# Performance work log

Measured on AMD Instinct MI355X. Metric: run time of the kernel, lower is better.

Reference implementation:

```python
import jax, jax.numpy as jnp
import numpy as np

N_NODES = 50000
N_EDGES = 500000
ATOM_DIM = 128
BOND_DIM = 64
EMB = 128
N_GRAPHS = 256
NUM_LAYER = 2


def _kaiming_uniform(key, fan_out, fan_in):
    # kaiming_uniform_ with nonlinearity='relu': bound = sqrt(6 / fan_in) * sqrt(2)/1 adjustments
    gain = np.sqrt(2.0)
    bound = gain * np.sqrt(3.0 / fan_in)
    return jax.random.uniform(key, (fan_out, fan_in), jnp.float32, -bound, bound)


def setup_inputs() -> dict:
    key = jax.random.key(0)
    ks = jax.random.split(key, 12)
    x = jax.random.normal(ks[0], (N_NODES, ATOM_DIM), jnp.float32)
    edge_attr = jax.random.normal(ks[1], (N_EDGES, BOND_DIM), jnp.float32)
    edge_index = jax.random.randint(ks[2], (2, N_EDGES), 0, N_NODES, jnp.int64)
    batch = jnp.sort(jax.random.randint(ks[3], (N_NODES,), 0, N_GRAPHS, jnp.int64))
    Wa = _kaiming_uniform(ks[4], EMB, ATOM_DIM)
    ba = jnp.zeros((EMB,), jnp.float32)
    Wb = _kaiming_uniform(ks[5], EMB, BOND_DIM)
    bb = jnp.zeros((EMB,), jnp.float32)
    W1 = _kaiming_uniform(ks[6], EMB, EMB)
    b1 = jnp.zeros((EMB,), jnp.float32)
    W2 = _kaiming_uniform(ks[7], EMB // 2, EMB)
    b2 = jnp.zeros((EMB // 2,), jnp.float32)
    W3 = _kaiming_uniform(ks[8], 1, EMB // 2)
    return {"x": x, "edge_attr": edge_attr, "edge_index": edge_index, "batch": batch,
            "Wa": Wa, "ba": ba, "Wb": Wb, "bb": bb,
            "W1": W1, "b1": b1, "W2": W2, "b2": b2, "W3": W3}


def reference(x, edge_attr, edge_index, batch, Wa, ba, Wb, bb, W1, b1, W2, b2, W3):
    src, dst = edge_index[0], edge_index[1]
    # Step 1: embeddings
    node_emb = x @ Wa.T + ba          # [N, EMB]
    edge_emb = edge_attr @ Wb.T + bb  # [E, EMB]
    # Step 2: message passing layers: gather, multiply with edge_emb, scatter-add, residual
    for _ in range(NUM_LAYER):
        msg = node_emb[src] * edge_emb                           # [E, EMB]
        agg = jax.ops.segment_sum(msg, dst, num_segments=N_NODES)  # [N, EMB]
        node_emb = node_emb + agg
    # Step 3: energy MLP (ReLU first, per nn.Sequential)
    h = jax.nn.relu(node_emb)
    h = jax.nn.relu(h @ W1.T + b1)
    h = jax.nn.relu(h @ W2.T + b2)
    node_energy = h @ W3.T            # [N, 1], no bias
    # Step 4: global add pool over graphs
    dg = jax.ops.segment_sum(node_energy, batch, num_segments=N_GRAPHS)  # [G, 1]
    return dg
```

## Files before the change

### kernel.cpp

```cpp
#include <hip/hip_runtime.h>
#include <cstdio>
#include <cstdint>

#define N_NODES 50000
#define N_EDGES 500000
#define EMB 128
#define BOND 64
#define NGRAPH 256
#define NB_SCAN ((N_NODES + 255) / 256)
#define NSTRIP (N_NODES / 16)
#define HSTR 136

typedef short bf16x8 __attribute__((ext_vector_type(8)));
typedef float f32x4  __attribute__((ext_vector_type(4)));

__device__ __forceinline__ unsigned short f2bf(float v){
  unsigned u = __float_as_uint(v);
  unsigned r = (u + 0x7fffu + ((u >> 16) & 1u)) >> 16;
  return (unsigned short)r;
}
__device__ __forceinline__ float bf2f(unsigned short u){
  return __uint_as_float(((unsigned)u) << 16);
}
__device__ __forceinline__ unsigned short brelu(unsigned short u){
  return (u & 0x8000u) ? (unsigned short)0 : u;
}

__global__ void prep_w(const float* __restrict__ Wa, const float* __restrict__ W1,
                       const float* __restrict__ W2, unsigned short* __restrict__ wabf,
                       unsigned short* __restrict__ w1bf, unsigned short* __restrict__ w2bf)
{
  int i = blockIdx.x * 256 + threadIdx.x;
  int i2 = i & 16383;
  int j = i2 & 7, lb = (i2 >> 3) & 63, kc = (i2 >> 9) & 3, tn = i2 >> 11;
  int lm = lb & 15, q = lb >> 4;
  int row = tn * 16 + lm, col = kc * 32 + q * 8 + j;
  if (i < 16384){
    wabf[i] = f2bf(Wa[row * EMB + col]);
  } else if (i < 32768){
    w1bf[i2] = f2bf(W1[row * EMB + col]);
  } else if (i < 32768 + 8192){
    w2bf[i2] = f2bf(W2[row * EMB + col]);
  }
}

__global__ __launch_bounds__(256) void node_gemm_mfma(const float* __restrict__ x,
    const unsigned short* __restrict__ wabf, const float* __restrict__ ba,
    unsigned short* __restrict__ out)
{
  __shared__ unsigned short hs[4][16 * HSTR];
  const int t = threadIdx.x;
  const int wv = t >> 6, l = t & 63;
  const int lm = l & 15, q = l >> 4;
  union U8 { bf16x8 v; unsigned short s[8]; };
  const int strip = blockIdx.x * 4 + wv;
  if (strip >= NSTRIP) return;
  const long n0 = (long)strip * 16;

  bf16x8 a[4];
  #pragma unroll
  for (int kc = 0; kc < 4; kc++){
    const float* ap = x + (n0 + lm) * (long)EMB + kc * 32 + q * 8;
    float4 x0 = *(const float4*)ap;
    float4 x1 = *(const float4*)(ap + 4);
    U8 u;
    u.s[0] = f2bf(x0.x); u.s[1] = f2bf(x0.y); u.s[2] = f2bf(x0.z); u.s[3] = f2bf(x0.w);
    u.s[4] = f2bf(x1.x); u.s[5] = f2bf(x1.y); u.s[6] = f2bf(x1.z); u.s[7] = f2bf(x1.w);
    a[kc] = u.v;
  }
  float biasv[8];
  #pragma unroll
  for (int tn = 0; tn < 8; tn++) biasv[tn] = ba[tn * 16 + lm];

  unsigned short* hw = hs[wv];
  #pragma unroll
  for (int tn = 0; tn < 8; tn++){
    f32x4 acc = {0.f, 0.f, 0.f, 0.f};
    #pragma unroll
    for (int kc = 0; kc < 4; kc++){
      bf16x8 bf = *(const bf16x8*)(wabf + (size_t)((tn * 4 + kc) * 64 + l) * 8);
      acc = __builtin_amdgcn_mfma_f32_16x16x32_bf16(a[kc], bf, acc, 0, 0, 0);
    }
    #pragma unroll
    for (int i = 0; i < 4; i++)
      hw[(q * 4 + i) * HSTR + tn * 16 + lm] = f2bf(acc[i] + biasv[tn]);
  }
  #pragma unroll
  for (int rb = 0; rb < 4; rb++){
    int row = rb * 4 + q;
    ushort4 v0 = *(const ushort4*)(hw + row * HSTR + lm * 8);
    ushort4 v1 = *(const ushort4*)(hw + row * HSTR + lm * 8 + 4);
    unsigned short* op = out + (n0 + row) * (long)EMB + lm * 8;
    *(ushort4*)op = v0;
    *(ushort4*)(op + 4) = v1;
  }
}

__global__ __launch_bounds__(128) void edge_gemm_mfma(
    const float* __restrict__ attr, const float* __restrict__ Wb,
    const float* __restrict__ bb, const int2* __restrict__ cse,
    unsigned short* __restrict__ eemb)
{
  __shared__ unsigned short hs[2][32 * HSTR];
  const int t = threadIdx.x;
  const int wv = t >> 6;
  const int l  = t & 63;
  const int lm = l & 15;
  const int q  = l >> 4;
  union U8 { bf16x8 v; unsigned short s[8]; };

  bf16x8 bfrag[8][2];
  float bias[8];
  #pragma unroll
  for (int tn = 0; tn < 8; tn++){
    bias[tn] = bb[tn * 16 + lm];
    #pragma unroll
    for (int h = 0; h < 2; h++){
      const float* wp = Wb + (tn * 16 + lm) * BOND + h * 32 + q * 8;
      float4 w0 = *(const float4*)wp;
      float4 w1 = *(const float4*)(wp + 4);
      U8 u;
      u.s[0] = f2bf(w0.x); u.s[1] = f2bf(w0.y); u.s[2] = f2bf(w0.z); u.s[3] = f2bf(w0.w);
      u.s[4] = f2bf(w1.x); u.s[5] = f2bf(w1.y); u.s[6] = f2bf(w1.z); u.s[7] = f2bf(w1.w);
      bfrag[tn][h] = u.v;
    }
  }

  unsigned short* hw = hs[wv];
  const long stride = (long)gridDim.x * 2 * 32;
  for (long p0 = ((long)blockIdx.x * 2 + wv) * 32; p0 < N_EDGES; p0 += stride){
    long eidA = (long)cse[p0 + lm].y;
    long eidB = (long)cse[p0 + 16 + lm].y;
    bf16x8 afA[2], afB[2];
    #pragma unroll
    for (int h = 0; h < 2; h++){
      const float* apA = attr + eidA * BOND + h * 32 + q * 8;
      const float* apB = attr + eidB * BOND + h * 32 + q * 8;
      float4 a0 = *(const float4*)apA;
      float4 a1 = *(const float4*)(apA + 4);
      float4 b0 = *(const float4*)apB;
      float4 b1 = *(const float4*)(apB + 4);
      U8 u;
      u.s[0] = f2bf(a0.x); u.s[1] = f2bf(a0.y); u.s[2] = f2bf(a0.z); u.s[3] = f2bf(a0.w);
      u.s[4] = f2bf(a1.x); u.s[5] = f2bf(a1.y); u.s[6] = f2bf(a1.z); u.s[7] = f2bf(a1.w);
      afA[h] = u.v;
      u.s[0] = f2bf(b0.x); u.s[1] = f2bf(b0.y); u.s[2] = f2bf(b0.z); u.s[3] = f2bf(b0.w);
      u.s[4] = f2bf(b1.x); u.s[5] = f2bf(b1.y); u.s[6] = f2bf(b1.z); u.s[7] = f2bf(b1.w);
      afB[h] = u.v;
    }
    #pragma unroll
    for (int tn = 0; tn < 8; tn++){
      f32x4 accA = {0.f, 0.f, 0.f, 0.f};
      f32x4 accB = {0.f, 0.f, 0.f, 0.f};
      accA = __builtin_amdgcn_mfma_f32_16x16x32_bf16(afA[0], bfrag[tn][0], accA, 0, 0, 0);
      accA = __builtin_amdgcn_mfma_f32_16x16x32_bf16(afA[1], bfrag[tn][1], accA, 0, 0, 0);
      accB = __builtin_amdgcn_mfma_f32_16x16x32_bf16(afB[0], bfrag[tn][0], accB, 0, 0, 0);
      accB = __builtin_amdgcn_mfma_f32_16x16x32_bf16(afB[1], bfrag[tn][1], accB, 0, 0, 0);
      #pragma unroll
      for (int i = 0; i < 4; i++){
        hw[(q * 4 + i) * HSTR + tn * 16 + lm]      = f2bf(accA[i] + bias[tn]);
        hw[(16 + q * 4 + i) * HSTR + tn * 16 + lm] = f2bf(accB[i] + bias[tn]);
      }
    }
    #pragma unroll
    for (int rb = 0; rb < 8; rb++){
      int row = rb * 4 + q;
      ushort4 v0 = *(const ushort4*)(hw + row * HSTR + lm * 8);
      ushort4 v1 = *(const ushort4*)(hw + row * HSTR + lm * 8 + 4);
      unsigned short* op = eemb + (p0 + row) * (long)EMB + lm * 8;
      *(ushort4*)op = v0;
      *(ushort4*)(op + 4) = v1;
    }
  }
}


__global__ __launch_bounds__(256) void count_deg(const int* __restrict__ ei,
                                                 int* __restrict__ deg)
{
  int e = blockIdx.x * 256 + threadIdx.x;
  if (e < N_EDGES) atomicAdd(&deg[ei[N_EDGES + e]], 1);
}

__global__ __launch_bounds__(256) void scan_s1(const int* __restrict__ deg,
                                               int* __restrict__ blocksum)
{
  int i = blockIdx.x * 256 + threadIdx.x;
  int lane = threadIdx.x & 63, w = threadIdx.x >> 6;
  int v = (i < N_NODES) ? deg[i] : 0;
  #pragma unroll
  for (int o = 32; o > 0; o >>= 1) v += __shfl_down(v, o, 64);
  __shared__ int ws4[4];
  if (lane == 0) ws4[w] = v;
  __syncthreads();
  if (threadIdx.x == 0) blocksum[blockIdx.x] = ws4[0] + ws4[1] + ws4[2] + ws4[3];
}

__global__ __launch_bounds__(256) void scan_s2(const int* __restrict__ blocksum,
                                               int* __restrict__ blockoff,
                                               int* __restrict__ off)
{
  int t = threadIdx.x;
  int lane = t & 63, w = t >> 6;
  int v = (t < NB_SCAN) ? blocksum[t] : 0;
  int x = v;
  #pragma unroll
  for (int d = 1; d < 64; d <<= 1){
    int y = __shfl_up(x, d, 64);
    if (lane >= d) x += y;
  }
  __shared__ int wsum[4];
  if (lane == 63) wsum[w] = x;
  __syncthreads();
  int wo = 0;
  for (int j = 0; j < w; j++) wo += wsum[j];
  if (t < NB_SCAN) blockoff[t] = wo + x - v;
  if (t == 0) off[N_NODES] = wsum[0] + wsum[1] + wsum[2] + wsum[3];
}

__global__ __launch_bounds__(256) void scan_s3(const int* __restrict__ deg,
    const int* __restrict__ blockoff, int* __restrict__ off, int* __restrict__ fill)
{
  int i = blockIdx.x * 256 + threadIdx.x;
  int lane = threadIdx.x & 63, w = threadIdx.x >> 6;
  int v = (i < N_NODES) ? deg[i] : 0;
  int x = v;
  #pragma unroll
  for (int d = 1; d < 64; d <<= 1){
    int y = __shfl_up(x, d, 64);
    if (lane >= d) x += y;
  }
  __shared__ int wsum[4];
  if (lane == 63) wsum[w] = x;
  __syncthreads();
  int wo = 0;
  for (int j = 0; j < w; j++) wo += wsum[j];
  if (i < N_NODES){
    int excl = blockoff[blockIdx.x] + wo + x - v;
    off[i] = excl;
    fill[i] = excl;
  }
}

__global__ __launch_bounds__(256) void scatter_edges(const int* __restrict__ ei,
    int* __restrict__ fill, int2* __restrict__ cse)
{
  int e = blockIdx.x * 256 + threadIdx.x;
  if (e < N_EDGES){
    int dst = ei[N_EDGES + e];
    int p = atomicAdd(&fill[dst], 1);
    cse[p] = make_int2(ei[e], e);
  }
}

__global__ __launch_bounds__(256) void agg_kernel(const unsigned short* __restrict__ node_old,
    const unsigned short* __restrict__ eemb, const int* __restrict__ off,
    const int2* __restrict__ cse, unsigned short* __restrict__ node_new)
{
  int n = blockIdx.x * 8 + (threadIdx.x >> 5);
  if (n >= N_NODES) return;
  int c0 = (threadIdx.x & 31) * 4;
  int s = off[n], e = off[n + 1];
  ushort4 r = *(const ushort4*)(node_old + (long)n * EMB + c0);
  float4 accA = make_float4(bf2f(r.x), bf2f(r.y), bf2f(r.z), bf2f(r.w));
  float4 accB = make_float4(0.f, 0.f, 0.f, 0.f);
  int i = s;
  for (; i + 8 <= e; i += 8){
    int idx[8];
    #pragma unroll
    for (int j = 0; j < 8; j++) idx[j] = cse[i + j].x;
    ushort4 a[8], eb[8];
    #pragma unroll
    for (int j = 0; j < 8; j++){
      a[j]  = *(const ushort4*)(node_old + (long)idx[j] * EMB + c0);
      eb[j] = *(const ushort4*)(eemb + (long)(i + j) * EMB + c0);
    }
    #pragma unroll
    for (int j = 0; j < 8; j++){
      float4& acc = (j & 1) ? accB : accA;
      acc.x = fmaf(bf2f(a[j].x), bf2f(eb[j].x), acc.x);
      acc.y = fmaf(bf2f(a[j].y), bf2f(eb[j].y), acc.y);
      acc.z = fmaf(bf2f(a[j].z), bf2f(eb[j].z), acc.z);
      acc.w = fmaf(bf2f(a[j].w), bf2f(eb[j].w), acc.w);
    }
  }
  for (; i < e; i++){
    int src = cse[i].x;
    ushort4 a  = *(const ushort4*)(node_old + (long)src * EMB + c0);
    ushort4 eb = *(const ushort4*)(eemb + (long)i * EMB + c0);
    accA.x = fmaf(bf2f(a.x), bf2f(eb.x), accA.x);
    accA.y = fmaf(bf2f(a.y), bf2f(eb.y), accA.y);
    accA.z = fmaf(bf2f(a.z), bf2f(eb.z), accA.z);
    accA.w = fmaf(bf2f(a.w), bf2f(eb.w), accA.w);
  }
  ushort4 o;
  o.x = f2bf(accA.x + accB.x);
  o.y = f2bf(accA.y + accB.y);
  o.z = f2bf(accA.z + accB.z);
  o.w = f2bf(accA.w + accB.w);
  *(ushort4*)(node_new + (long)n * EMB + c0) = o;
}

__global__ __launch_bounds__(256) void mlp_mfma_pool(const unsigned short* __restrict__ ne,
    const unsigned short* __restrict__ w1bf, const unsigned short* __restrict__ w2bf,
    const float* __restrict__ b1, const float* __restrict__ b2,
    const float* __restrict__ W3, const int* __restrict__ batch,
    float* __restrict__ dg)
{
  __shared__ float h1s[4][16 * 132];
  __shared__ float pool[NGRAPH];
  const int t = threadIdx.x;
  const int wv = t >> 6, l = t & 63;
  const int lm = l & 15, q = l >> 4;
  union U8 { bf16x8 v; unsigned short s[8]; };

  for (int i = t; i < NGRAPH; i += 256) pool[i] = 0.f;
  __syncthreads();

  const int strip = blockIdx.x * 4 + wv;
  if (strip < NSTRIP){
    const long n0 = (long)strip * 16;

    float b1v[8], b2v[4], w3v[4];
    #pragma unroll
    for (int tn = 0; tn < 8; tn++) b1v[tn] = b1[tn * 16 + lm];
    #pragma unroll
    for (int tc = 0; tc < 4; tc++){ b2v[tc] = b2[tc * 16 + lm]; w3v[tc] = W3[tc * 16 + lm]; }

    bf16x8 a1[4];
    #pragma unroll
    for (int kc = 0; kc < 4; kc++){
      const unsigned short* ap = ne + (n0 + lm) * (long)EMB + kc * 32 + q * 8;
      ushort4 v0 = *(const ushort4*)ap;
      ushort4 v1 = *(const ushort4*)(ap + 4);
      U8 u;
      u.s[0] = brelu(v0.x); u.s[1] = brelu(v0.y); u.s[2] = brelu(v0.z); u.s[3] = brelu(v0.w);
      u.s[4] = brelu(v1.x); u.s[5] = brelu(v1.y); u.s[6] = brelu(v1.z); u.s[7] = brelu(v1.w);
      a1[kc] = u.v;
    }

    f32x4 acc1[8];
    #pragma unroll
    for (int tn = 0; tn < 8; tn++) acc1[tn] = (f32x4){b1v[tn], b1v[tn], b1v[tn], b1v[tn]};
    #pragma unroll
    for (int kc = 0; kc < 4; kc++){
      #pragma unroll
      for (int tn = 0; tn < 8; tn++){
        bf16x8 bf = *(const bf16x8*)(w1bf + (size_t)((tn * 4 + kc) * 64 + l) * 8);
        acc1[tn] = __builtin_amdgcn_mfma_f32_16x16x32_bf16(a1[kc], bf, acc1[tn], 0, 0, 0);
      }
    }

    float* h1 = h1s[wv];
    #pragma unroll
    for (int tn = 0; tn < 8; tn++)
      #pragma unroll
      for (int i = 0; i < 4; i++)
        h1[(q * 4 + i) * 132 + tn * 16 + lm] = fmaxf(acc1[tn][i], 0.f);
    bf16x8 a2[4];
    #pragma unroll
    for (int kc = 0; kc < 4; kc++){
      const float* hp = h1 + lm * 132 + kc * 32 + q * 8;
      float4 x0 = *(const float4*)hp;
      float4 x1 = *(const float4*)(hp + 4);
      U8 u;
      u.s[0] = f2bf(x0.x); u.s[1] = f2bf(x0.y); u.s[2] = f2bf(x0.z); u.s[3] = f2bf(x0.w);
      u.s[4] = f2bf(x1.x); u.s[5] = f2bf(x1.y); u.s[6] = f2bf(x1.z); u.s[7] = f2bf(x1.w);
      a2[kc] = u.v;
    }

    f32x4 acc2[4];
    #pragma unroll
    for (int tc = 0; tc < 4; tc++) acc2[tc] = (f32x4){b2v[tc], b2v[tc], b2v[tc], b2v[tc]};
    #pragma unroll
    for (int kc = 0; kc < 4; kc++){
      #pragma unroll
      for (int tc = 0; tc < 4; tc++){
        bf16x8 bf = *(const bf16x8*)(w2bf + (size_t)((tc * 4 + kc) * 64 + l) * 8);
        acc2[tc] = __builtin_amdgcn_mfma_f32_16x16x32_bf16(a2[kc], bf, acc2[tc], 0, 0, 0);
      }
    }

    float e4[4];
    #pragma unroll
    for (int i = 0; i < 4; i++){
      float s = 0.f;
      #pragma unroll
      for (int tc = 0; tc < 4; tc++) s = fmaf(fmaxf(acc2[tc][i], 0.f), w3v[tc], s);
      e4[i] = s;
    }
    #pragma unroll
    for (int m = 1; m < 16; m <<= 1)
      #pragma unroll
      for (int i = 0; i < 4; i++) e4[i] += __shfl_xor(e4[i], m, 64);
    if (lm == 0){
      #pragma unroll
      for (int i = 0; i < 4; i++){
        int node = (int)n0 + q * 4 + i;
        atomicAdd(&pool[batch[node]], e4[i]);
      }
    }
  }
  __syncthreads();
  for (int i = t; i < NGRAPH; i += 256){
    float v = pool[i];
    if (v != 0.f) atomicAdd(&dg[i], v);
  }
}

extern "C" void kernel_launch(void* const* d_in, const int* in_sizes, int n_in,
                              void* d_out, int out_size, void* d_ws, size_t ws_size,
                              hipStream_t stream)
{
  const float* x         = (const float*)d_in[0];
  const float* edge_attr = (const float*)d_in[1];
  const int*   ei        = (const int*)d_in[2];
  const int*   batch     = (const int*)d_in[3];
  const float* Wa = (const float*)d_in[4];
  const float* ba = (const float*)d_in[5];
  const float* Wb = (const float*)d_in[6];
  const float* bb = (const float*)d_in[7];
  const float* W1 = (const float*)d_in[8];
  const float* b1 = (const float*)d_in[9];
  const float* W2 = (const float*)d_in[10];
  const float* b2 = (const float*)d_in[11];
  const float* W3 = (const float*)d_in[12];

  char* ws = (char*)d_ws;
  size_t p = 0;
  auto alloc = [&](size_t bytes) -> char* {
    char* q = ws + p;
    p += (bytes + 255) & ~(size_t)255;
    return q;
  };
  unsigned short* bufA = (unsigned short*)alloc((size_t)N_NODES * EMB * 2);
  unsigned short* bufB = (unsigned short*)alloc((size_t)N_NODES * EMB * 2);
  unsigned short* eemb = (unsigned short*)alloc((size_t)N_EDGES * EMB * 2);
  unsigned short* wabf = (unsigned short*)alloc(16384 * sizeof(short));
  unsigned short* w1bf = (unsigned short*)alloc(16384 * sizeof(short));
  unsigned short* w2bf = (unsigned short*)alloc(8192 * sizeof(short));
  int* deg  = (int*)alloc(N_NODES * sizeof(int));
  int* off  = (int*)alloc((N_NODES + 1) * sizeof(int));
  int* fill = (int*)alloc(N_NODES * sizeof(int));
  int* blocksum = (int*)alloc(NB_SCAN * sizeof(int));
  int* blockoff = (int*)alloc(NB_SCAN * sizeof(int));
  int2* cse = (int2*)alloc((size_t)N_EDGES * sizeof(int2));
  if (p > ws_size){
    fprintf(stderr, "kernel_launch: ws too small (%zu < %zu)\n", ws_size, p);
    return;
  }

  hipMemsetAsync(deg, 0, N_NODES * sizeof(int), stream);
  count_deg<<<(N_EDGES + 255) / 256, 256, 0, stream>>>(ei, deg);
  scan_s1<<<NB_SCAN, 256, 0, stream>>>(deg, blocksum);
  scan_s2<<<1, 256, 0, stream>>>(blocksum, blockoff, off);
  scan_s3<<<NB_SCAN, 256, 0, stream>>>(deg, blockoff, off, fill);
  scatter_edges<<<(N_EDGES + 255) / 256, 256, 0, stream>>>(ei, fill, cse);

  prep_w<<<160, 256, 0, stream>>>(Wa, W1, W2, wabf, w1bf, w2bf);
  node_gemm_mfma<<<(NSTRIP + 3) / 4, 256, 0, stream>>>(x, wabf, ba, bufA);
  edge_gemm_mfma<<<2048, 128, 0, stream>>>(edge_attr, Wb, bb, cse, eemb);

  agg_kernel<<<(N_NODES + 7) / 8, 256, 0, stream>>>(bufA, eemb, off, cse, bufB);
  agg_kernel<<<(N_NODES + 7) / 8, 256, 0, stream>>>(bufB, eemb, off, cse, bufA);

  hipMemsetAsync(d_out, 0, NGRAPH * sizeof(float), stream);
  mlp_mfma_pool<<<(NSTRIP + 3) / 4, 256, 0, stream>>>(bufA, w1bf, w2bf, b1, b2, W3, batch, (float*)d_out);
}
```

Baseline: 434.4 us.

## Store embeddings in permuted column order to drop LDS transpose staging

The node and edge GEMM kernels now write MFMA accumulators straight to global memory as 16-byte vectors. Each lane packs its 8 column tiles, so stored embeddings use a permuted column order. W1 is pre-permuted in prep_w to match, and the elementwise gather/multiply/scatter in aggregation is unaffected by the permutation. This removes the per-wave shared-memory round trip and its LDS traffic. The edge GEMM also loads a pre-converted bf16 Wb and processes 16 edges per wave with 4 waves per block, which trades per-wave reuse for more parallelism.

```diff
diff --git a/kernel.cpp b/kernel.cpp
--- a/kernel.cpp
+++ b/kernel.cpp
@@ -9,7 +9,7 @@
 #define NGRAPH 256
 #define NB_SCAN ((N_NODES + 255) / 256)
 #define NSTRIP (N_NODES / 16)
-#define HSTR 136
+#define ESTRIP (N_EDGES / 16)
 
 typedef short bf16x8 __attribute__((ext_vector_type(8)));
 typedef float f32x4  __attribute__((ext_vector_type(4)));
@@ -26,21 +26,31 @@
   return (u & 0x8000u) ? (unsigned short)0 : u;
 }
 
+
 __global__ void prep_w(const float* __restrict__ Wa, const float* __restrict__ W1,
-                       const float* __restrict__ W2, unsigned short* __restrict__ wabf,
-                       unsigned short* __restrict__ w1bf, unsigned short* __restrict__ w2bf)
+                       const float* __restrict__ W2, const float* __restrict__ Wb,
+                       unsigned short* __restrict__ wabf, unsigned short* __restrict__ w1bf,
+                       unsigned short* __restrict__ w2bf, unsigned short* __restrict__ wbbf)
 {
   int i = blockIdx.x * 256 + threadIdx.x;
-  int i2 = i & 16383;
-  int j = i2 & 7, lb = (i2 >> 3) & 63, kc = (i2 >> 9) & 3, tn = i2 >> 11;
-  int lm = lb & 15, q = lb >> 4;
-  int row = tn * 16 + lm, col = kc * 32 + q * 8 + j;
-  if (i < 16384){
-    wabf[i] = f2bf(Wa[row * EMB + col]);
-  } else if (i < 32768){
-    w1bf[i2] = f2bf(W1[row * EMB + col]);
-  } else if (i < 32768 + 8192){
-    w2bf[i2] = f2bf(W2[row * EMB + col]);
+  if (i < 40960){
+    int i2 = i & 16383;
+    int j = i2 & 7, lb = (i2 >> 3) & 63, kc = (i2 >> 9) & 3, tn = i2 >> 11;
+    int lm = lb & 15, q = lb >> 4;
+    int row = tn * 16 + lm, col = kc * 32 + q * 8 + j;
+    if (i < 16384){
+      wabf[i] = f2bf(Wa[row * EMB + col]);
+    } else if (i < 32768){
+      int pcol = j * 16 + kc * 4 + q;
+      w1bf[i2] = f2bf(W1[row * EMB + pcol]);
+    } else {
+      w2bf[i2] = f2bf(W2[row * EMB + col]);
+    }
+  } else if (i < 49152){
+    int i2 = i - 40960;
+    int j = i2 & 7, l = (i2 >> 3) & 63, kc = (i2 >> 9) & 1, tn = i2 >> 10;
+    int lm = l & 15, q = l >> 4;
+    wbbf[i2] = f2bf(Wb[(tn * 16 + lm) * BOND + kc * 32 + q * 8 + j]);
   }
 }
 
@@ -48,7 +58,6 @@
     const unsigned short* __restrict__ wabf, const float* __restrict__ ba,
     unsigned short* __restrict__ out)
 {
-  __shared__ unsigned short hs[4][16 * HSTR];
   const int t = threadIdx.x;
   const int wv = t >> 6, l = t & 63;
   const int lm = l & 15, q = l >> 4;
@@ -72,41 +81,34 @@
   #pragma unroll
   for (int tn = 0; tn < 8; tn++) biasv[tn] = ba[tn * 16 + lm];
 
-  unsigned short* hw = hs[wv];
-  #pragma unroll
-  for (int tn = 0; tn < 8; tn++){
-    f32x4 acc = {0.f, 0.f, 0.f, 0.f};
-    #pragma unroll
-    for (int kc = 0; kc < 4; kc++){
+  f32x4 acc[8];
+  #pragma unroll
+  for (int tn = 0; tn < 8; tn++) acc[tn] = (f32x4){0.f, 0.f, 0.f, 0.f};
+  #pragma unroll
+  for (int kc = 0; kc < 4; kc++){
+    #pragma unroll
+    for (int tn = 0; tn < 8; tn++){
       bf16x8 bf = *(const bf16x8*)(wabf + (size_t)((tn * 4 + kc) * 64 + l) * 8);
-      acc = __builtin_amdgcn_mfma_f32_16x16x32_bf16(a[kc], bf, acc, 0, 0, 0);
-    }
-    #pragma unroll
-    for (int i = 0; i < 4; i++)
-      hw[(q * 4 + i) * HSTR + tn * 16 + lm] = f2bf(acc[i] + biasv[tn]);
-  }
-  #pragma unroll
-  for (int rb = 0; rb < 4; rb++){
-    int row = rb * 4 + q;
-    ushort4 v0 = *(const ushort4*)(hw + row * HSTR + lm * 8);
-    ushort4 v1 = *(const ushort4*)(hw + row * HSTR + lm * 8 + 4);
-    unsigned short* op = out + (n0 + row) * (long)EMB + lm * 8;
-    *(ushort4*)op = v0;
-    *(ushort4*)(op + 4) = v1;
-  }
-}
-
-__global__ __launch_bounds__(128) void edge_gemm_mfma(
-    const float* __restrict__ attr, const float* __restrict__ Wb,
+      acc[tn] = __builtin_amdgcn_mfma_f32_16x16x32_bf16(a[kc], bf, acc[tn], 0, 0, 0);
+    }
+  }
+  #pragma unroll
+  for (int i = 0; i < 4; i++){
+    U8 o;
+    #pragma unroll
+    for (int tn = 0; tn < 8; tn++) o.s[tn] = f2bf(acc[tn][i] + biasv[tn]);
+    *(bf16x8*)(out + (n0 + q * 4 + i) * (long)EMB + lm * 8) = o.v;
+  }
+}
+
+__global__ __launch_bounds__(256) void edge_gemm_mfma(
+    const float* __restrict__ attr, const unsigned short* __restrict__ wbbf,
     const float* __restrict__ bb, const int2* __restrict__ cse,
     unsigned short* __restrict__ eemb)
 {
-  __shared__ unsigned short hs[2][32 * HSTR];
   const int t = threadIdx.x;
-  const int wv = t >> 6;
-  const int l  = t & 63;
-  const int lm = l & 15;
-  const int q  = l >> 4;
+  const int l = t & 63;
+  const int lm = l & 15, q = l >> 4;
   union U8 { bf16x8 v; unsigned short s[8]; };
 
   bf16x8 bfrag[8][2];
@@ -115,61 +117,40 @@
   for (int tn = 0; tn < 8; tn++){
     bias[tn] = bb[tn * 16 + lm];
     #pragma unroll
-    for (int h = 0; h < 2; h++){
-      const float* wp = Wb + (tn * 16 + lm) * BOND + h * 32 + q * 8;
-      float4 w0 = *(const float4*)wp;
-      float4 w1 = *(const float4*)(wp + 4);
-      U8 u;
-      u.s[0] = f2bf(w0.x); u.s[1] = f2bf(w0.y); u.s[2] = f2bf(w0.z); u.s[3] = f2bf(w0.w);
-      u.s[4] = f2bf(w1.x); u.s[5] = f2bf(w1.y); u.s[6] = f2bf(w1.z); u.s[7] = f2bf(w1.w);
-      bfrag[tn][h] = u.v;
-    }
-  }
-
-  unsigned short* hw = hs[wv];
-  const long stride = (long)gridDim.x * 2 * 32;
-  for (long p0 = ((long)blockIdx.x * 2 + wv) * 32; p0 < N_EDGES; p0 += stride){
-    long eidA = (long)cse[p0 + lm].y;
-    long eidB = (long)cse[p0 + 16 + lm].y;
-    bf16x8 afA[2], afB[2];
-    #pragma unroll
-    for (int h = 0; h < 2; h++){
-      const float* apA = attr + eidA * BOND + h * 32 + q * 8;
-      const float* apB = attr + eidB * BOND + h * 32 + q * 8;
-      float4 a0 = *(const float4*)apA;
-      float4 a1 = *(const float4*)(apA + 4);
-      float4 b0 = *(const float4*)apB;
-      float4 b1 = *(const float4*)(apB + 4);
+    for (int kc = 0; kc < 2; kc++)
+      bfrag[tn][kc] = *(const bf16x8*)(wbbf + (size_t)((tn * 2 + kc) * 64 + l) * 8);
+  }
+
+  const long wid = (long)blockIdx.x * 4 + (t >> 6);
+  const long stride = (long)gridDim.x * 4 * 16;
+  for (long p0 = wid * 16; p0 < N_EDGES; p0 += stride){
+    long eid = (long)cse[p0 + lm].y;
+    bf16x8 af[2];
+    #pragma unroll
+    for (int kc = 0; kc < 2; kc++){
+      const float* ap = attr + eid * BOND + kc * 32 + q * 8;
+      float4 a0 = *(const float4*)ap;
+      float4 a1 = *(const float4*)(ap + 4);
       U8 u;
       u.s[0] = f2bf(a0.x); u.s[1] = f2bf(a0.y); u.s[2] = f2bf(a0.z); u.s[3] = f2bf(a0.w);
       u.s[4] = f2bf(a1.x); u.s[5] = f2bf(a1.y); u.s[6] = f2bf(a1.z); u.s[7] = f2bf(a1.w);
-      afA[h] = u.v;
-      u.s[0] = f2bf(b0.x); u.s[1] = f2bf(b0.y); u.s[2] = f2bf(b0.z); u.s[3] = f2bf(b0.w);
-      u.s[4] = f2bf(b1.x); u.s[5] = f2bf(b1.y); u.s[6] = f2bf(b1.z); u.s[7] = f2bf(b1.w);
-      afB[h] = u.v;
-    }
-    #pragma unroll
-    for (int tn = 0; tn < 8; tn++){
-      f32x4 accA = {0.f, 0.f, 0.f, 0.f};
-      f32x4 accB = {0.f, 0.f, 0.f, 0.f};
-      accA = __builtin_amdgcn_mfma_f32_16x16x32_bf16(afA[0], bfrag[tn][0], accA, 0, 0, 0);
-      accA = __builtin_amdgcn_mfma_f32_16x16x32_bf16(afA[1], bfrag[tn][1], accA, 0, 0, 0);
-      accB = __builtin_amdgcn_mfma_f32_16x16x32_bf16(afB[0], bfrag[tn][0], accB, 0, 0, 0);
-      accB = __builtin_amdgcn_mfma_f32_16x16x32_bf16(afB[1], bfrag[tn][1], accB, 0, 0, 0);
-      #pragma unroll
-      for (int i = 0; i < 4; i++){
-        hw[(q * 4 + i) * HSTR + tn * 16 + lm]      = f2bf(accA[i] + bias[tn]);
-        hw[(16 + q * 4 + i) * HSTR + tn * 16 + lm] = f2bf(accB[i] + bias[tn]);
-      }
-    }
-    #pragma unroll
-    for (int rb = 0; rb < 8; rb++){
-      int row = rb * 4 + q;
-      ushort4 v0 = *(const ushort4*)(hw + row * HSTR + lm * 8);
-      ushort4 v1 = *(const ushort4*)(hw + row * HSTR + lm * 8 + 4);
-      unsigned short* op = eemb + (p0 + row) * (long)EMB + lm * 8;
-      *(ushort4*)op = v0;
-      *(ushort4*)(op + 4) = v1;
+      af[kc] = u.v;
+    }
+    f32x4 acc[8];
+    #pragma unroll
+    for (int tn = 0; tn < 8; tn++) acc[tn] = (f32x4){0.f, 0.f, 0.f, 0.f};
+    #pragma unroll
+    for (int kc = 0; kc < 2; kc++){
+      #pragma unroll
+      for (int tn = 0; tn < 8; tn++)
+        acc[tn] = __builtin_amdgcn_mfma_f32_16x16x32_bf16(af[kc], bfrag[tn][kc], acc[tn], 0, 0, 0);
+    }
+    #pragma unroll
+    for (int i = 0; i < 4; i++){
+      U8 o;
+      #pragma unroll
+      for (int tn = 0; tn < 8; tn++) o.s[tn] = f2bf(acc[tn][i] + bias[tn]);
+      *(bf16x8*)(eemb + (p0 + q * 4 + i) * (long)EMB + lm * 8) = o.v;
     }
   }
 }
@@ -439,6 +420,7 @@
   unsigned short* wabf = (unsigned short*)alloc(16384 * sizeof(short));
   unsigned short* w1bf = (unsigned short*)alloc(16384 * sizeof(short));
   unsigned short* w2bf = (unsigned short*)alloc(8192 * sizeof(short));
+  unsigned short* wbbf = (unsigned short*)alloc(8192 * sizeof(short));
   int* deg  = (int*)alloc(N_NODES * sizeof(int));
   int* off  = (int*)alloc((N_NODES + 1) * sizeof(int));
   int* fill = (int*)alloc(N_NODES * sizeof(int));
@@ -457,9 +439,9 @@
   scan_s3<<<NB_SCAN, 256, 0, stream>>>(deg, blockoff, off, fill);
   scatter_edges<<<(N_EDGES + 255) / 256, 256, 0, stream>>>(ei, fill, cse);
 
-  prep_w<<<160, 256, 0, stream>>>(Wa, W1, W2, wabf, w1bf, w2bf);
+  prep_w<<<192, 256, 0, stream>>>(Wa, W1, W2, Wb, wabf, w1bf, w2bf, wbbf);
   node_gemm_mfma<<<(NSTRIP + 3) / 4, 256, 0, stream>>>(x, wabf, ba, bufA);
-  edge_gemm_mfma<<<2048, 128, 0, stream>>>(edge_attr, Wb, bb, cse, eemb);
+  edge_gemm_mfma<<<2048, 256, 0, stream>>>(edge_attr, wbbf, bb, cse, eemb);
 
   agg_kernel<<<(N_NODES + 7) / 8, 256, 0, stream>>>(bufA, eemb, off, cse, bufB);
   agg_kernel<<<(N_NODES + 7) / 8, 256, 0, stream>>>(bufB, eemb, off, cse, bufA);
```

New measurement: 428.1 us. About the same (-1.4%).
